# Kernel tuning notes

Measured on AMD Instinct MI355X. Metric: run time of the kernel, lower is better.

The kernel has to match this reference:

```python
import jax, jax.numpy as jnp
import numpy as np

B, S, HID = 1, 4096, 1024
HQ, HKV, D = 16, 4, 64   # query heads, kv heads (GQA), dim_per_head
ROPE_BASE = 10000.0


def setup_inputs() -> dict:
    key = jax.random.key(0)
    ks = jax.random.split(key, 5)
    s = 0.02
    return {
        "x": jax.random.normal(ks[0], (B, S, HID), jnp.float32),
        "Wq": jax.random.normal(ks[1], (HID, HQ * D), jnp.float32) * s,
        "Wk": jax.random.normal(ks[2], (HID, HKV * D), jnp.float32) * s,
        "Wv": jax.random.normal(ks[3], (HID, HKV * D), jnp.float32) * s,
        "Wo": jax.random.normal(ks[4], (HQ * D, HID), jnp.float32) * s,
    }


def _rope(t, cos, sin):
    # non-interleaved (half-split) rotary; t: [B,S,H,D], cos/sin: [S, D//2]
    t1, t2 = jnp.split(t, 2, axis=-1)
    c = cos[None, :, None, :]
    sn = sin[None, :, None, :]
    return jnp.concatenate([t1 * c - t2 * sn, t2 * c + t1 * sn], axis=-1)


def reference(x, Wq, Wk, Wv, Wo):
    # QKV projections (self-attention: key=value=query=x), reshape to [B,S,H,D]
    q = (x @ Wq).reshape(B, S, HQ, D)
    k = (x @ Wk).reshape(B, S, HKV, D)
    v = (x @ Wv).reshape(B, S, HKV, D)

    # rotary position embedding over full head dim
    inv_freq = 1.0 / (ROPE_BASE ** (jnp.arange(0, D, 2, dtype=jnp.float32) / D))
    ang = jnp.arange(S, dtype=jnp.float32)[:, None] * inv_freq[None, :]  # [S, D//2]
    cos, sin = jnp.cos(ang), jnp.sin(ang)
    q = _rope(q, cos, sin)
    k = _rope(k, cos, sin)

    # GQA: expand kv heads to match query heads
    g = HQ // HKV
    k = jnp.repeat(k, g, axis=2)
    v = jnp.repeat(v, g, axis=2)

    scale = D ** -0.5  # attn_scaling ** -0.5 with attn_scaling = dim_per_head
    scores = jnp.einsum('bqhd,bkhd->bhqk', q, k) * scale  # [B,HQ,S,S]
    causal = jnp.tril(jnp.ones((S, S), dtype=bool))
    scores = jnp.where(causal[None, None], scores, jnp.finfo(scores.dtype).min)
    attn = jax.nn.softmax(scores, axis=-1)

    ctx = jnp.einsum('bhqk,bkhd->bqhd', attn, v).reshape(B, S, HQ * D)
    return ctx @ Wo
```

## Files before the change

### kernel.cpp

```cpp
#include <hip/hip_runtime.h>
#include <hip/hip_bf16.h>
#include <math.h>

typedef __attribute__((ext_vector_type(8))) short short8;
typedef __attribute__((ext_vector_type(4))) float f32x4;

#define S_   4096
#define HQ_  16
#define HKV_ 4
#define D_   64

static __device__ __forceinline__ unsigned short f2b(float f) {
    __hip_bfloat16 h = __float2bfloat16(f);
    return *reinterpret_cast<unsigned short*>(&h);
}
static __device__ __forceinline__ float b2f(unsigned short u) {
    union { unsigned int u; float f; } c;
    c.u = ((unsigned int)u) << 16;
    return c.f;
}

typedef __attribute__((address_space(1))) const unsigned int gas_u32;
typedef __attribute__((address_space(3))) unsigned int las_u32;
static __device__ __forceinline__ void gload16(const void* g, void* l) {
    __builtin_amdgcn_global_load_lds((gas_u32*)g, (las_u32*)l, 16, 0, 0);
}


__global__ __launch_bounds__(256) void k_prep(const float* __restrict__ Wq,
                                              const float* __restrict__ Wk,
                                              const float* __restrict__ Wv,
                                              const float* __restrict__ Wo,
                                              const float* __restrict__ x,
                                              unsigned short* __restrict__ WT,
                                              unsigned short* __restrict__ WoT,
                                              unsigned short* __restrict__ xb,
                                              float* __restrict__ cs) {
    const int z = blockIdx.z;
    const int t = threadIdx.x;
    if (z == 4) {
        int flat = blockIdx.y * 32 + blockIdx.x;
#pragma unroll
        for (int ii = 0; ii < 4; ++ii) {
            int i = flat * 1024 + ii * 256 + t;
            float4 v = ((const float4*)x)[i];
            ushort4 o;
            o.x = f2b(v.x); o.y = f2b(v.y); o.z = f2b(v.z); o.w = f2b(v.w);
            ((ushort4*)xb)[i] = o;
        }
        return;
    }
    if (z == 5) {
        int flat = blockIdx.y * 32 + blockIdx.x;
        if (flat >= 512) return;
        int i = flat * 256 + t;
        int s = i >> 5, jj = i & 31;
        float invf = exp2f(-(float)jj * (13.287712379549449f / 32.0f));
        float ang = (float)s * invf;
        ((float2*)cs)[i] = make_float2(cosf(ang), sinf(ang));
        return;
    }
    const float* tin; unsigned short* tout; int N, gx;
    if (z == 0)      { tin = Wq; tout = WT;                 N = 1024; gx = 32; }
    else if (z == 1) { tin = Wk; tout = WT + 1024 * 1024;   N = 256;  gx = 8;  }
    else if (z == 2) { tin = Wv; tout = WT + 1280 * 1024;   N = 256;  gx = 8;  }
    else             { tin = Wo; tout = WoT;                N = 1024; gx = 32; }
    if ((int)blockIdx.x >= gx) return;
    __shared__ float tile[32][33];
    int tx = t & 31, ty = t >> 5;
    int n0 = blockIdx.x * 32, k0 = blockIdx.y * 32;
#pragma unroll
    for (int r = 0; r < 32; r += 8)
        tile[ty + r][tx] = tin[(size_t)(k0 + ty + r) * N + n0 + tx];
    __syncthreads();
#pragma unroll
    for (int r = 0; r < 32; r += 8)
        tout[(size_t)(n0 + ty + r) * 1024 + k0 + tx] = f2b(tile[tx][ty + r]);
}


__global__ __launch_bounds__(256, 3)
void k_gemm_qkv(const unsigned short* __restrict__ A,
                const unsigned short* __restrict__ BT,
                const float* __restrict__ cs,
                unsigned short* __restrict__ Qr,
                unsigned short* __restrict__ Kr,
                unsigned short* __restrict__ Vp) {
    __shared__ unsigned short As[2][128 * 64];
    __shared__ unsigned short Bs[2][64 * 64];
    const int t = threadIdx.x;
    const int ntile = blockIdx.x;
    const int n0 = ntile * 64;
    const int m0 = blockIdx.y * 128;
    const int w = t >> 6, lane = t & 63, lr = lane & 15, lg = lane >> 4;
    const int sr = lane >> 3, sch = (lane & 7) * 16;
    const int K = 1024;

    f32x4 acc[2][4];
#pragma unroll
    for (int m = 0; m < 2; ++m)
#pragma unroll
        for (int n = 0; n < 4; ++n) acc[m][n] = (f32x4){0.f, 0.f, 0.f, 0.f};

    auto stage = [&](int buf, int k0) {
#pragma unroll
        for (int c = 0; c < 4; ++c) {
            int r0 = w * 32 + c * 8;
            int r = r0 + sr;
            gload16((const char*)&A[(size_t)(m0 + r) * K + k0] + (sch ^ ((r & 7) << 4)),
                    (char*)&As[buf][0] + r0 * 128);
        }
#pragma unroll
        for (int c = 0; c < 2; ++c) {
            int r0 = w * 16 + c * 8;
            int r = r0 + sr;
            gload16((const char*)&BT[(size_t)(n0 + r) * K + k0] + (sch ^ ((r & 7) << 4)),
                    (char*)&Bs[buf][0] + r0 * 128);
        }
    };

    int cur = 0;
    stage(0, 0);
    __syncthreads();

    for (int k0 = 0; k0 < K; k0 += 64) {
        if (k0 + 64 < K) stage(cur ^ 1, k0 + 64);
        const char* AsB = (const char*)&As[cur][0];
        const char* BsB = (const char*)&Bs[cur][0];
        __builtin_amdgcn_s_setprio(1);
#pragma unroll
        for (int kk = 0; kk < 2; ++kk) {
            short8 af[2], bf[4];
#pragma unroll
            for (int m = 0; m < 2; ++m) {
                int arow = w * 32 + m * 16 + lr;
                af[m] = *(const short8*)(AsB + arow * 128 +
                                         ((kk * 64 + lg * 16) ^ ((arow & 7) << 4)));
            }
#pragma unroll
            for (int n = 0; n < 4; ++n) {
                int brow = n * 16 + lr;
                bf[n] = *(const short8*)(BsB + brow * 128 +
                                         ((kk * 64 + lg * 16) ^ ((brow & 7) << 4)));
            }
#pragma unroll
            for (int m = 0; m < 2; ++m)
#pragma unroll
                for (int n = 0; n < 4; ++n)
                    acc[m][n] = __builtin_amdgcn_mfma_f32_16x16x32_bf16(af[m], bf[n], acc[m][n], 0, 0, 0);
        }
        __builtin_amdgcn_s_setprio(0);
        __syncthreads();
        cur ^= 1;
    }

    if (ntile < 20) {
        const float QS = (ntile < 16) ? 0.125f * 1.44269504088896340736f : 1.0f;
        unsigned short* dst = (ntile < 16) ? (Qr + (size_t)ntile * (S_ * D_))
                                           : (Kr + (size_t)(ntile - 16) * (S_ * D_));
#pragma unroll
        for (int m = 0; m < 2; ++m)
#pragma unroll
            for (int rr = 0; rr < 4; ++rr) {
                int s = m0 + w * 32 + m * 16 + lg * 4 + rr;
                const float2* csr = (const float2*)cs + s * 32;
                float2 c0 = csr[lr];
                float2 c1 = csr[16 + lr];
                float t1 = acc[m][0][rr], t2 = acc[m][2][rr];
                dst[(size_t)s * 64 + lr]      = f2b((t1 * c0.x - t2 * c0.y) * QS);
                dst[(size_t)s * 64 + 32 + lr] = f2b((t2 * c0.x + t1 * c0.y) * QS);
                t1 = acc[m][1][rr]; t2 = acc[m][3][rr];
                dst[(size_t)s * 64 + 16 + lr] = f2b((t1 * c1.x - t2 * c1.y) * QS);
                dst[(size_t)s * 64 + 48 + lr] = f2b((t2 * c1.x + t1 * c1.y) * QS);
            }
    } else {
        int h2 = ntile - 20;
        unsigned short* dst = Vp + (size_t)h2 * (D_ * S_);
#pragma unroll
        for (int m = 0; m < 2; ++m)
#pragma unroll
            for (int n = 0; n < 4; ++n) {
                int d = n * 16 + lr;
                int pos = m0 + (w >> 1) * 64 + (w & 1) * 32 + lg * 8 + m * 4;
                ushort4 o;
                o.x = f2b(acc[m][n][0]); o.y = f2b(acc[m][n][1]);
                o.z = f2b(acc[m][n][2]); o.w = f2b(acc[m][n][3]);
                *(ushort4*)&dst[(size_t)d * S_ + pos] = o;
            }
    }
}


__global__ __launch_bounds__(256, 3)
void k_gemm_o(const unsigned short* __restrict__ A,
              const unsigned short* __restrict__ BT,
              float* __restrict__ out) {
    __shared__ unsigned short As[2][128 * 64];
    __shared__ unsigned short Bs[2][64 * 64];
    const int t = threadIdx.x;
    const int n0 = blockIdx.x * 64;
    const int m0 = blockIdx.y * 128;
    const int w = t >> 6, lane = t & 63, lr = lane & 15, lg = lane >> 4;
    const int sr = lane >> 3, sch = (lane & 7) * 16;
    const int K = 1024;

    f32x4 acc[2][4];
#pragma unroll
    for (int m = 0; m < 2; ++m)
#pragma unroll
        for (int n = 0; n < 4; ++n) acc[m][n] = (f32x4){0.f, 0.f, 0.f, 0.f};

    auto stage = [&](int buf, int k0) {
#pragma unroll
        for (int c = 0; c < 4; ++c) {
            int r0 = w * 32 + c * 8;
            int r = r0 + sr;
            gload16((const char*)&A[(size_t)(m0 + r) * K + k0] + (sch ^ ((r & 7) << 4)),
                    (char*)&As[buf][0] + r0 * 128);
        }
#pragma unroll
        for (int c = 0; c < 2; ++c) {
            int r0 = w * 16 + c * 8;
            int r = r0 + sr;
            gload16((const char*)&BT[(size_t)(n0 + r) * K + k0] + (sch ^ ((r & 7) << 4)),
                    (char*)&Bs[buf][0] + r0 * 128);
        }
    };

    int cur = 0;
    stage(0, 0);
    __syncthreads();

    for (int k0 = 0; k0 < K; k0 += 64) {
        if (k0 + 64 < K) stage(cur ^ 1, k0 + 64);
        const char* AsB = (const char*)&As[cur][0];
        const char* BsB = (const char*)&Bs[cur][0];
        __builtin_amdgcn_s_setprio(1);
#pragma unroll
        for (int kk = 0; kk < 2; ++kk) {
            short8 af[2], bf[4];
#pragma unroll
            for (int m = 0; m < 2; ++m) {
                int arow = w * 32 + m * 16 + lr;
                af[m] = *(const short8*)(AsB + arow * 128 +
                                         ((kk * 64 + lg * 16) ^ ((arow & 7) << 4)));
            }
#pragma unroll
            for (int n = 0; n < 4; ++n) {
                int brow = n * 16 + lr;
                bf[n] = *(const short8*)(BsB + brow * 128 +
                                         ((kk * 64 + lg * 16) ^ ((brow & 7) << 4)));
            }
#pragma unroll
            for (int m = 0; m < 2; ++m)
#pragma unroll
                for (int n = 0; n < 4; ++n)
                    acc[m][n] = __builtin_amdgcn_mfma_f32_16x16x32_bf16(af[m], bf[n], acc[m][n], 0, 0, 0);
        }
        __builtin_amdgcn_s_setprio(0);
        __syncthreads();
        cur ^= 1;
    }
#pragma unroll
    for (int m = 0; m < 2; ++m)
#pragma unroll
        for (int n = 0; n < 4; ++n)
#pragma unroll
            for (int rr = 0; rr < 4; ++rr) {
                int row = m0 + w * 32 + m * 16 + lg * 4 + rr;
                int col = n0 + n * 16 + lr;
                out[(size_t)row * 1024 + col] = acc[m][n][rr];
            }
}


__global__ __launch_bounds__(256, 4)
void k_attn(const unsigned short* __restrict__ Qr,
            const unsigned short* __restrict__ Kr,
            const unsigned short* __restrict__ Vp,
            unsigned short* __restrict__ Pacc,
            float* __restrict__ Psv) {
    __shared__ unsigned short Ks[2][64 * 64];
    __shared__ unsigned short Vs[2][64 * 64];

    const int t = threadIdx.x;
    const int p = blockIdx.x;
    const int h = blockIdx.y;
    const int j = blockIdx.z;
    const int kvh = h >> 2;
    const int w = t >> 6, lane = t & 63, lr = lane & 15, lg = lane >> 4;

    const unsigned short* Qh = Qr + (size_t)h * (S_ * D_);
    const unsigned short* Kh = Kr + (size_t)kvh * (S_ * D_);
    const unsigned short* Vh = Vp + (size_t)kvh * (D_ * S_);

    const int xw = (lr & 7) << 4;
    const int sr = lane >> 3, sch = (lane & 7) * 16;
    const int r0a = w * 16, r0b = w * 16 + 8;

#pragma unroll 1
    for (int half = 0; half < 2; ++half) {
        const int qb = half ? p : (63 - p);
        const int tend = qb + 1;
        const int qi = qb * 64 + w * 16 + lr;

        const char* kp[2];
        const char* vp[2];
        {
            int ra = r0a + sr, rb = r0b + sr;
            kp[0] = (const char*)(Kh + (size_t)(j * 64 + ra) * 64) + (sch ^ ((ra & 7) << 4));
            kp[1] = (const char*)(Kh + (size_t)(j * 64 + rb) * 64) + (sch ^ ((rb & 7) << 4));
            vp[0] = (const char*)(Vh + (size_t)ra * S_ + j * 64) + (sch ^ ((ra & 7) << 4));
            vp[1] = (const char*)(Vh + (size_t)rb * S_ + j * 64) + (sch ^ ((rb & 7) << 4));
        }
        auto stage = [&](int buf) {
            gload16(kp[0], (char*)&Ks[buf][0] + r0a * 128);
            gload16(kp[1], (char*)&Ks[buf][0] + r0b * 128);
            gload16(vp[0], (char*)&Vs[buf][0] + r0a * 128);
            gload16(vp[1], (char*)&Vs[buf][0] + r0b * 128);
            kp[0] += 16384; kp[1] += 16384;
            vp[0] += 256;   vp[1] += 256;
        };

        short8 aq[2];
        {
            int qrow = qb * 64 + w * 16 + lr;
            aq[0] = *(const short8*)&Qh[(size_t)qrow * 64 + lg * 8];
            aq[1] = *(const short8*)&Qh[(size_t)qrow * 64 + 32 + lg * 8];
        }
        float svl = 0.f;
        f32x4 acc_o[4];
#pragma unroll
        for (int i = 0; i < 4; ++i) acc_o[i] = (f32x4){0.f, 0.f, 0.f, 0.f};

        int cur = 0;
        stage(0);
        __syncthreads();

        for (int kb = j; kb < tend; kb += 2) {
            if (kb + 2 < tend) stage(cur ^ 1);

            f32x4 s[4];
#pragma unroll
            for (int i = 0; i < 4; ++i) s[i] = (f32x4){0.f, 0.f, 0.f, 0.f};
            const char* KsB = (const char*)&Ks[cur][0];
            __builtin_amdgcn_s_setprio(1);
#pragma unroll
            for (int kk = 0; kk < 2; ++kk)
#pragma unroll
                for (int nt = 0; nt < 4; ++nt) {
                    short8 kf = *(const short8*)(KsB + (nt * 16 + lr) * 128 + ((kk * 64 + lg * 16) ^ xw));
                    s[nt] = __builtin_amdgcn_mfma_f32_16x16x32_bf16(kf, aq[kk], s[nt], 0, 0, 0);
                }
            __builtin_amdgcn_s_setprio(0);

            if (kb == qb) {
                int kbase = kb * 64 + lg * 4;
#pragma unroll
                for (int nt = 0; nt < 4; ++nt)
#pragma unroll
                    for (int rr = 0; rr < 4; ++rr)
                        if (kbase + nt * 16 + rr > qi) s[nt][rr] = -INFINITY;
            }

            unsigned int wd[8];
#pragma unroll
            for (int nt = 0; nt < 4; ++nt) {
                float p0 = exp2f(s[nt][0]), p1 = exp2f(s[nt][1]);
                float p2 = exp2f(s[nt][2]), p3 = exp2f(s[nt][3]);
                svl += (p0 + p1) + (p2 + p3);
                asm("v_cvt_pk_bf16_f32 %0, %1, %2" : "=v"(wd[nt * 2])     : "v"(p0), "v"(p1));
                asm("v_cvt_pk_bf16_f32 %0, %1, %2" : "=v"(wd[nt * 2 + 1]) : "v"(p2), "v"(p3));
            }

            const char* VsB = (const char*)&Vs[cur][0];
            __builtin_amdgcn_s_setprio(1);
#pragma unroll
            for (int kk = 0; kk < 2; ++kk) {
                union { unsigned int u[4]; short8 s8; } pa;
                pa.u[0] = wd[4 * kk + 0]; pa.u[1] = wd[4 * kk + 1];
                pa.u[2] = wd[4 * kk + 2]; pa.u[3] = wd[4 * kk + 3];
#pragma unroll
                for (int nt = 0; nt < 4; ++nt) {
                    short8 vb = *(const short8*)(VsB + (nt * 16 + lr) * 128 + ((kk * 64 + lg * 16) ^ xw));
                    acc_o[nt] = __builtin_amdgcn_mfma_f32_16x16x32_bf16(pa.s8, vb, acc_o[nt], 0, 0, 0);
                }
            }
            __builtin_amdgcn_s_setprio(0);

            __syncthreads();
            cur ^= 1;
        }

        svl += __shfl_xor(svl, 16);
        svl += __shfl_xor(svl, 32);
        const int u = ((j * 64 + qb) * 16 + h);
        if (lg == 0) Psv[u * 64 + w * 16 + lr] = svl;
        unsigned short* Pb = Pacc + (size_t)u * 4096;
#pragma unroll
        for (int nt = 0; nt < 4; ++nt) {
            int rr = w * 16 + lg * 4;
            int col = nt * 16 + lr;
            Pb[(rr + 0) * 64 + col] = f2b(acc_o[nt][0]);
            Pb[(rr + 1) * 64 + col] = f2b(acc_o[nt][1]);
            Pb[(rr + 2) * 64 + col] = f2b(acc_o[nt][2]);
            Pb[(rr + 3) * 64 + col] = f2b(acc_o[nt][3]);
        }
    }
}


__global__ __launch_bounds__(256) void k_combine(const unsigned short* __restrict__ Pacc,
                                                 const float* __restrict__ Psv,
                                                 unsigned short* __restrict__ O) {
    const int qb = blockIdx.x, h = blockIdx.y;
    const int t = threadIdx.x;
    const int r = t >> 2, db = (t & 3) * 16;
    const int u0 = (qb * 16 + h);
    const int u1 = ((64 + qb) * 16 + h);
    float sa = Psv[u0 * 64 + r], sb = Psv[u1 * 64 + r];
    float inv = 1.f / (sa + sb);
    const unsigned short* A_ = Pacc + (size_t)u0 * 4096 + r * 64 + db;
    const unsigned short* B_ = Pacc + (size_t)u1 * 4096 + r * 64 + db;
    unsigned short* Op = O + (size_t)(qb * 64 + r) * 1024 + h * 64 + db;
#pragma unroll
    for (int halfv = 0; halfv < 2; ++halfv) {
        short8 va = *(const short8*)(A_ + halfv * 8);
        short8 vb = *(const short8*)(B_ + halfv * 8);
        short8 o;
#pragma unroll
        for (int i = 0; i < 8; ++i)
            o[i] = (short)f2b((b2f((unsigned short)va[i]) + b2f((unsigned short)vb[i])) * inv);
        *(short8*)(Op + halfv * 8) = o;
    }
}


extern "C" void kernel_launch(void* const* d_in, const int* in_sizes, int n_in,
                              void* d_out, int out_size, void* d_ws, size_t ws_size,
                              hipStream_t stream) {
    const float* x  = (const float*)d_in[0];
    const float* Wq = (const float*)d_in[1];
    const float* Wk = (const float*)d_in[2];
    const float* Wv = (const float*)d_in[3];
    const float* Wo = (const float*)d_in[4];
    float* out = (float*)d_out;
    char* ws = (char*)d_ws;

    unsigned short* WT  = (unsigned short*)(ws + 0);
    unsigned short* WoT = (unsigned short*)(ws + 3145728);
    unsigned short* Qr  = (unsigned short*)(ws + 5242880);
    unsigned short* Kr  = (unsigned short*)(ws + 13631488);
    unsigned short* Vp  = (unsigned short*)(ws + 15728640);
    unsigned short* O   = (unsigned short*)(ws + 17825792);
    float* cs           = (float*)(ws + 26214400);
    unsigned short* xb  = (unsigned short*)(ws + 27262976);
    unsigned short* Pacc = (unsigned short*)(ws + 27262976);
    float* Psv           = (float*)(ws + 44040192);

    k_prep<<<dim3(32, 32, 6), 256, 0, stream>>>(Wq, Wk, Wv, Wo, x, WT, WoT, xb, cs);
    k_gemm_qkv<<<dim3(24, 32), 256, 0, stream>>>(xb, WT, cs, Qr, Kr, Vp);
    k_attn<<<dim3(32, 16, 2), 256, 0, stream>>>(Qr, Kr, Vp, Pacc, Psv);
    k_combine<<<dim3(64, 16), 256, 0, stream>>>(Pacc, Psv, O);
    k_gemm_o<<<dim3(16, 32), 256, 0, stream>>>(O, WoT, out);
}
```

Measured before the change: 114.6 us.

## Fuse split-KV combine into output projection GEMM A-tile loading

Removes the separate combine kernel and instead has the output-projection GEMM read both split-KV partial accumulators and their row sums directly. It normalizes them in registers and writes the combined bf16 tile into shared memory. This saves one kernel launch and a round trip of the intermediate O buffer through global memory. The cost is that A-tile staging becomes register-mediated rather than async direct-to-LDS, and each K-step now does extra loads and arithmetic. The attention kernel is only moved in the file.

```diff
diff --git a/kernel.cpp b/kernel.cpp
--- a/kernel.cpp
+++ b/kernel.cpp
@@ -191,8 +191,145 @@
 }
 
 
+__global__ __launch_bounds__(256, 4)
+void k_attn(const unsigned short* __restrict__ Qr,
+            const unsigned short* __restrict__ Kr,
+            const unsigned short* __restrict__ Vp,
+            unsigned short* __restrict__ Pacc,
+            float* __restrict__ Psv) {
+    __shared__ unsigned short Ks[2][64 * 64];
+    __shared__ unsigned short Vs[2][64 * 64];
+
+    const int t = threadIdx.x;
+    const int p = blockIdx.x;
+    const int h = blockIdx.y;
+    const int j = blockIdx.z;
+    const int kvh = h >> 2;
+    const int w = t >> 6, lane = t & 63, lr = lane & 15, lg = lane >> 4;
+
+    const unsigned short* Qh = Qr + (size_t)h * (S_ * D_);
+    const unsigned short* Kh = Kr + (size_t)kvh * (S_ * D_);
+    const unsigned short* Vh = Vp + (size_t)kvh * (D_ * S_);
+
+    const int xw = (lr & 7) << 4;
+    const int sr = lane >> 3, sch = (lane & 7) * 16;
+    const int r0a = w * 16, r0b = w * 16 + 8;
+
+#pragma unroll 1
+    for (int half = 0; half < 2; ++half) {
+        const int qb = half ? p : (63 - p);
+        const int tend = qb + 1;
+        const int qi = qb * 64 + w * 16 + lr;
+
+        const char* kp[2];
+        const char* vp[2];
+        {
+            int ra = r0a + sr, rb = r0b + sr;
+            kp[0] = (const char*)(Kh + (size_t)(j * 64 + ra) * 64) + (sch ^ ((ra & 7) << 4));
+            kp[1] = (const char*)(Kh + (size_t)(j * 64 + rb) * 64) + (sch ^ ((rb & 7) << 4));
+            vp[0] = (const char*)(Vh + (size_t)ra * S_ + j * 64) + (sch ^ ((ra & 7) << 4));
+            vp[1] = (const char*)(Vh + (size_t)rb * S_ + j * 64) + (sch ^ ((rb & 7) << 4));
+        }
+        auto stage = [&](int buf) {
+            gload16(kp[0], (char*)&Ks[buf][0] + r0a * 128);
+            gload16(kp[1], (char*)&Ks[buf][0] + r0b * 128);
+            gload16(vp[0], (char*)&Vs[buf][0] + r0a * 128);
+            gload16(vp[1], (char*)&Vs[buf][0] + r0b * 128);
+            kp[0] += 16384; kp[1] += 16384;
+            vp[0] += 256;   vp[1] += 256;
+        };
+
+        short8 aq[2];
+        {
+            int qrow = qb * 64 + w * 16 + lr;
+            aq[0] = *(const short8*)&Qh[(size_t)qrow * 64 + lg * 8];
+            aq[1] = *(const short8*)&Qh[(size_t)qrow * 64 + 32 + lg * 8];
+        }
+        float svl = 0.f;
+        f32x4 acc_o[4];
+#pragma unroll
+        for (int i = 0; i < 4; ++i) acc_o[i] = (f32x4){0.f, 0.f, 0.f, 0.f};
+
+        int cur = 0;
+        stage(0);
+        __syncthreads();
+
+        for (int kb = j; kb < tend; kb += 2) {
+            if (kb + 2 < tend) stage(cur ^ 1);
+
+            f32x4 s[4];
+#pragma unroll
+            for (int i = 0; i < 4; ++i) s[i] = (f32x4){0.f, 0.f, 0.f, 0.f};
+            const char* KsB = (const char*)&Ks[cur][0];
+            __builtin_amdgcn_s_setprio(1);
+#pragma unroll
+            for (int kk = 0; kk < 2; ++kk)
+#pragma unroll
+                for (int nt = 0; nt < 4; ++nt) {
+                    short8 kf = *(const short8*)(KsB + (nt * 16 + lr) * 128 + ((kk * 64 + lg * 16) ^ xw));
+                    s[nt] = __builtin_amdgcn_mfma_f32_16x16x32_bf16(kf, aq[kk], s[nt], 0, 0, 0);
+                }
+            __builtin_amdgcn_s_setprio(0);
+
+            if (kb == qb) {
+                int kbase = kb * 64 + lg * 4;
+#pragma unroll
+                for (int nt = 0; nt < 4; ++nt)
+#pragma unroll
+                    for (int rr = 0; rr < 4; ++rr)
+                        if (kbase + nt * 16 + rr > qi) s[nt][rr] = -INFINITY;
+            }
+
+            unsigned int wd[8];
+#pragma unroll
+            for (int nt = 0; nt < 4; ++nt) {
+                float p0 = exp2f(s[nt][0]), p1 = exp2f(s[nt][1]);
+                float p2 = exp2f(s[nt][2]), p3 = exp2f(s[nt][3]);
+                svl += (p0 + p1) + (p2 + p3);
+                asm("v_cvt_pk_bf16_f32 %0, %1, %2" : "=v"(wd[nt * 2])     : "v"(p0), "v"(p1));
+                asm("v_cvt_pk_bf16_f32 %0, %1, %2" : "=v"(wd[nt * 2 + 1]) : "v"(p2), "v"(p3));
+            }
+
+            const char* VsB = (const char*)&Vs[cur][0];
+            __builtin_amdgcn_s_setprio(1);
+#pragma unroll
+            for (int kk = 0; kk < 2; ++kk) {
+                union { unsigned int u[4]; short8 s8; } pa;
+                pa.u[0] = wd[4 * kk + 0]; pa.u[1] = wd[4 * kk + 1];
+                pa.u[2] = wd[4 * kk + 2]; pa.u[3] = wd[4 * kk + 3];
+#pragma unroll
+                for (int nt = 0; nt < 4; ++nt) {
+                    short8 vb = *(const short8*)(VsB + (nt * 16 + lr) * 128 + ((kk * 64 + lg * 16) ^ xw));
+                    acc_o[nt] = __builtin_amdgcn_mfma_f32_16x16x32_bf16(pa.s8, vb, acc_o[nt], 0, 0, 0);
+                }
+            }
+            __builtin_amdgcn_s_setprio(0);
+
+            __syncthreads();
+            cur ^= 1;
+        }
+
+        svl += __shfl_xor(svl, 16);
+        svl += __shfl_xor(svl, 32);
+        const int u = ((j * 64 + qb) * 16 + h);
+        if (lg == 0) Psv[u * 64 + w * 16 + lr] = svl;
+        unsigned short* Pb = Pacc + (size_t)u * 4096;
+#pragma unroll
+        for (int nt = 0; nt < 4; ++nt) {
+            int rr = w * 16 + lg * 4;
+            int col = nt * 16 + lr;
+            Pb[(rr + 0) * 64 + col] = f2b(acc_o[nt][0]);
+            Pb[(rr + 1) * 64 + col] = f2b(acc_o[nt][1]);
+            Pb[(rr + 2) * 64 + col] = f2b(acc_o[nt][2]);
+            Pb[(rr + 3) * 64 + col] = f2b(acc_o[nt][3]);
+        }
+    }
+}
+
+
 __global__ __launch_bounds__(256, 3)
-void k_gemm_o(const unsigned short* __restrict__ A,
+void k_gemm_o(const unsigned short* __restrict__ Pacc,
+              const float* __restrict__ Psv,
               const unsigned short* __restrict__ BT,
               float* __restrict__ out) {
     __shared__ unsigned short As[2][128 * 64];
@@ -202,7 +339,6 @@
     const int m0 = blockIdx.y * 128;
     const int w = t >> 6, lane = t & 63, lr = lane & 15, lg = lane >> 4;
     const int sr = lane >> 3, sch = (lane & 7) * 16;
-    const int K = 1024;
 
     f32x4 acc[2][4];
 #pragma unroll
@@ -210,29 +346,59 @@
 #pragma unroll
         for (int n = 0; n < 4; ++n) acc[m][n] = (f32x4){0.f, 0.f, 0.f, 0.f};
 
-    auto stage = [&](int buf, int k0) {
+    int4 a0[4], a1[4];
+    float svs[4];
+
+    auto issueA = [&](int ks) {
 #pragma unroll
         for (int c = 0; c < 4; ++c) {
-            int r0 = w * 32 + c * 8;
-            int r = r0 + sr;
-            gload16((const char*)&A[(size_t)(m0 + r) * K + k0] + (sch ^ ((r & 7) << 4)),
-                    (char*)&As[buf][0] + r0 * 128);
-        }
+            int r = w * 32 + c * 8 + sr;
+            int s = m0 + r;
+            int row6 = s & 63, qbb = s >> 6;
+            int u0 = qbb * 16 + ks;
+            int u1 = (64 + qbb) * 16 + ks;
+            a0[c] = *(const int4*)((const char*)(Pacc + (size_t)u0 * 4096 + row6 * 64) + sch);
+            a1[c] = *(const int4*)((const char*)(Pacc + (size_t)u1 * 4096 + row6 * 64) + sch);
+            svs[c] = Psv[u0 * 64 + row6] + Psv[u1 * 64 + row6];
+        }
+    };
+    auto writeA = [&](int buf) {
+#pragma unroll
+        for (int c = 0; c < 4; ++c) {
+            int r = w * 32 + c * 8 + sr;
+            float inv = 1.0f / svs[c];
+            const unsigned short* e0 = (const unsigned short*)&a0[c];
+            const unsigned short* e1 = (const unsigned short*)&a1[c];
+            unsigned int wds[4];
+#pragma unroll
+            for (int i = 0; i < 4; ++i) {
+                float x0 = (b2f(e0[2 * i])     + b2f(e1[2 * i]))     * inv;
+                float x1 = (b2f(e0[2 * i + 1]) + b2f(e1[2 * i + 1])) * inv;
+                asm("v_cvt_pk_bf16_f32 %0, %1, %2" : "=v"(wds[i]) : "v"(x0), "v"(x1));
+            }
+            int4 pk;
+            pk.x = (int)wds[0]; pk.y = (int)wds[1]; pk.z = (int)wds[2]; pk.w = (int)wds[3];
+            *(int4*)((char*)&As[buf][0] + r * 128 + (sch ^ ((r & 7) << 4))) = pk;
+        }
+    };
+    auto stageB = [&](int buf, int ks) {
 #pragma unroll
         for (int c = 0; c < 2; ++c) {
             int r0 = w * 16 + c * 8;
             int r = r0 + sr;
-            gload16((const char*)&BT[(size_t)(n0 + r) * K + k0] + (sch ^ ((r & 7) << 4)),
+            gload16((const char*)&BT[(size_t)(n0 + r) * 1024 + ks * 64] + (sch ^ ((r & 7) << 4)),
                     (char*)&Bs[buf][0] + r0 * 128);
         }
     };
 
     int cur = 0;
-    stage(0, 0);
+    issueA(0);
+    stageB(0, 0);
+    writeA(0);
     __syncthreads();
 
-    for (int k0 = 0; k0 < K; k0 += 64) {
-        if (k0 + 64 < K) stage(cur ^ 1, k0 + 64);
+    for (int ks = 0; ks < 16; ++ks) {
+        if (ks + 1 < 16) { issueA(ks + 1); stageB(cur ^ 1, ks + 1); }
         const char* AsB = (const char*)&As[cur][0];
         const char* BsB = (const char*)&Bs[cur][0];
         __builtin_amdgcn_s_setprio(1);
@@ -258,6 +424,7 @@
                     acc[m][n] = __builtin_amdgcn_mfma_f32_16x16x32_bf16(af[m], bf[n], acc[m][n], 0, 0, 0);
         }
         __builtin_amdgcn_s_setprio(0);
+        if (ks + 1 < 16) writeA(cur ^ 1);
         __syncthreads();
         cur ^= 1;
     }
@@ -271,168 +438,6 @@
                 int col = n0 + n * 16 + lr;
                 out[(size_t)row * 1024 + col] = acc[m][n][rr];
             }
-}
-
-
-__global__ __launch_bounds__(256, 4)
-void k_attn(const unsigned short* __restrict__ Qr,
-            const unsigned short* __restrict__ Kr,
-            const unsigned short* __restrict__ Vp,
-            unsigned short* __restrict__ Pacc,
-            float* __restrict__ Psv) {
-    __shared__ unsigned short Ks[2][64 * 64];
-    __shared__ unsigned short Vs[2][64 * 64];
-
-    const int t = threadIdx.x;
-    const int p = blockIdx.x;
-    const int h = blockIdx.y;
-    const int j = blockIdx.z;
-    const int kvh = h >> 2;
-    const int w = t >> 6, lane = t & 63, lr = lane & 15, lg = lane >> 4;
-
-    const unsigned short* Qh = Qr + (size_t)h * (S_ * D_);
-    const unsigned short* Kh = Kr + (size_t)kvh * (S_ * D_);
-    const unsigned short* Vh = Vp + (size_t)kvh * (D_ * S_);
-
-    const int xw = (lr & 7) << 4;
-    const int sr = lane >> 3, sch = (lane & 7) * 16;
-    const int r0a = w * 16, r0b = w * 16 + 8;
-
-#pragma unroll 1
-    for (int half = 0; half < 2; ++half) {
-        const int qb = half ? p : (63 - p);
-        const int tend = qb + 1;
-        const int qi = qb * 64 + w * 16 + lr;
-
-        const char* kp[2];
-        const char* vp[2];
-        {
-            int ra = r0a + sr, rb = r0b + sr;
-            kp[0] = (const char*)(Kh + (size_t)(j * 64 + ra) * 64) + (sch ^ ((ra & 7) << 4));
-            kp[1] = (const char*)(Kh + (size_t)(j * 64 + rb) * 64) + (sch ^ ((rb & 7) << 4));
-            vp[0] = (const char*)(Vh + (size_t)ra * S_ + j * 64) + (sch ^ ((ra & 7) << 4));
-            vp[1] = (const char*)(Vh + (size_t)rb * S_ + j * 64) + (sch ^ ((rb & 7) << 4));
-        }
-        auto stage = [&](int buf) {
-            gload16(kp[0], (char*)&Ks[buf][0] + r0a * 128);
-            gload16(kp[1], (char*)&Ks[buf][0] + r0b * 128);
-            gload16(vp[0], (char*)&Vs[buf][0] + r0a * 128);
-            gload16(vp[1], (char*)&Vs[buf][0] + r0b * 128);
-            kp[0] += 16384; kp[1] += 16384;
-            vp[0] += 256;   vp[1] += 256;
-        };
-
-        short8 aq[2];
-        {
-            int qrow = qb * 64 + w * 16 + lr;
-            aq[0] = *(const short8*)&Qh[(size_t)qrow * 64 + lg * 8];
-            aq[1] = *(const short8*)&Qh[(size_t)qrow * 64 + 32 + lg * 8];
-        }
-        float svl = 0.f;
-        f32x4 acc_o[4];
-#pragma unroll
-        for (int i = 0; i < 4; ++i) acc_o[i] = (f32x4){0.f, 0.f, 0.f, 0.f};
-
-        int cur = 0;
-        stage(0);
-        __syncthreads();
-
-        for (int kb = j; kb < tend; kb += 2) {
-            if (kb + 2 < tend) stage(cur ^ 1);
-
-            f32x4 s[4];
-#pragma unroll
-            for (int i = 0; i < 4; ++i) s[i] = (f32x4){0.f, 0.f, 0.f, 0.f};
-            const char* KsB = (const char*)&Ks[cur][0];
-            __builtin_amdgcn_s_setprio(1);
-#pragma unroll
-            for (int kk = 0; kk < 2; ++kk)
-#pragma unroll
-                for (int nt = 0; nt < 4; ++nt) {
-                    short8 kf = *(const short8*)(KsB + (nt * 16 + lr) * 128 + ((kk * 64 + lg * 16) ^ xw));
-                    s[nt] = __builtin_amdgcn_mfma_f32_16x16x32_bf16(kf, aq[kk], s[nt], 0, 0, 0);
-                }
-            __builtin_amdgcn_s_setprio(0);
-
-            if (kb == qb) {
-                int kbase = kb * 64 + lg * 4;
-#pragma unroll
-                for (int nt = 0; nt < 4; ++nt)
-#pragma unroll
-                    for (int rr = 0; rr < 4; ++rr)
-                        if (kbase + nt * 16 + rr > qi) s[nt][rr] = -INFINITY;
-            }
-
-            unsigned int wd[8];
-#pragma unroll
-            for (int nt = 0; nt < 4; ++nt) {
-                float p0 = exp2f(s[nt][0]), p1 = exp2f(s[nt][1]);
-                float p2 = exp2f(s[nt][2]), p3 = exp2f(s[nt][3]);
-                svl += (p0 + p1) + (p2 + p3);
-                asm("v_cvt_pk_bf16_f32 %0, %1, %2" : "=v"(wd[nt * 2])     : "v"(p0), "v"(p1));
-                asm("v_cvt_pk_bf16_f32 %0, %1, %2" : "=v"(wd[nt * 2 + 1]) : "v"(p2), "v"(p3));
-            }
-
-            const char* VsB = (const char*)&Vs[cur][0];
-            __builtin_amdgcn_s_setprio(1);
-#pragma unroll
-            for (int kk = 0; kk < 2; ++kk) {
-                union { unsigned int u[4]; short8 s8; } pa;
-                pa.u[0] = wd[4 * kk + 0]; pa.u[1] = wd[4 * kk + 1];
-                pa.u[2] = wd[4 * kk + 2]; pa.u[3] = wd[4 * kk + 3];
-#pragma unroll
-                for (int nt = 0; nt < 4; ++nt) {
-                    short8 vb = *(const short8*)(VsB + (nt * 16 + lr) * 128 + ((kk * 64 + lg * 16) ^ xw));
-                    acc_o[nt] = __builtin_amdgcn_mfma_f32_16x16x32_bf16(pa.s8, vb, acc_o[nt], 0, 0, 0);
-                }
-            }
-            __builtin_amdgcn_s_setprio(0);
-
-            __syncthreads();
-            cur ^= 1;
-        }
-
-        svl += __shfl_xor(svl, 16);
-        svl += __shfl_xor(svl, 32);
-        const int u = ((j * 64 + qb) * 16 + h);
-        if (lg == 0) Psv[u * 64 + w * 16 + lr] = svl;
-        unsigned short* Pb = Pacc + (size_t)u * 4096;
-#pragma unroll
-        for (int nt = 0; nt < 4; ++nt) {
-            int rr = w * 16 + lg * 4;
-            int col = nt * 16 + lr;
-            Pb[(rr + 0) * 64 + col] = f2b(acc_o[nt][0]);
-            Pb[(rr + 1) * 64 + col] = f2b(acc_o[nt][1]);
-            Pb[(rr + 2) * 64 + col] = f2b(acc_o[nt][2]);
-            Pb[(rr + 3) * 64 + col] = f2b(acc_o[nt][3]);
-        }
-    }
-}
-
-
-__global__ __launch_bounds__(256) void k_combine(const unsigned short* __restrict__ Pacc,
-                                                 const float* __restrict__ Psv,
-                                                 unsigned short* __restrict__ O) {
-    const int qb = blockIdx.x, h = blockIdx.y;
-    const int t = threadIdx.x;
-    const int r = t >> 2, db = (t & 3) * 16;
-    const int u0 = (qb * 16 + h);
-    const int u1 = ((64 + qb) * 16 + h);
-    float sa = Psv[u0 * 64 + r], sb = Psv[u1 * 64 + r];
-    float inv = 1.f / (sa + sb);
-    const unsigned short* A_ = Pacc + (size_t)u0 * 4096 + r * 64 + db;
-    const unsigned short* B_ = Pacc + (size_t)u1 * 4096 + r * 64 + db;
-    unsigned short* Op = O + (size_t)(qb * 64 + r) * 1024 + h * 64 + db;
-#pragma unroll
-    for (int halfv = 0; halfv < 2; ++halfv) {
-        short8 va = *(const short8*)(A_ + halfv * 8);
-        short8 vb = *(const short8*)(B_ + halfv * 8);
-        short8 o;
-#pragma unroll
-        for (int i = 0; i < 8; ++i)
-            o[i] = (short)f2b((b2f((unsigned short)va[i]) + b2f((unsigned short)vb[i])) * inv);
-        *(short8*)(Op + halfv * 8) = o;
-    }
 }
 
 
@@ -452,7 +457,6 @@
     unsigned short* Qr  = (unsigned short*)(ws + 5242880);
     unsigned short* Kr  = (unsigned short*)(ws + 13631488);
     unsigned short* Vp  = (unsigned short*)(ws + 15728640);
-    unsigned short* O   = (unsigned short*)(ws + 17825792);
     float* cs           = (float*)(ws + 26214400);
     unsigned short* xb  = (unsigned short*)(ws + 27262976);
     unsigned short* Pacc = (unsigned short*)(ws + 27262976);
@@ -461,6 +465,5 @@
     k_prep<<<dim3(32, 32, 6), 256, 0, stream>>>(Wq, Wk, Wv, Wo, x, WT, WoT, xb, cs);
     k_gemm_qkv<<<dim3(24, 32), 256, 0, stream>>>(xb, WT, cs, Qr, Kr, Vp);
     k_attn<<<dim3(32, 16, 2), 256, 0, stream>>>(Qr, Kr, Vp, Pacc, Psv);
-    k_combine<<<dim3(64, 16), 256, 0, stream>>>(Pacc, Psv, O);
-    k_gemm_o<<<dim3(16, 32), 256, 0, stream>>>(O, WoT, out);
-}
+    k_gemm_o<<<dim3(16, 32), 256, 0, stream>>>(Pacc, Psv, WoT, out);
+}
```

Measured after the change: 128.0 us. +11.7%, slower.
